# Kernel tuning notes

Measured on AMD Instinct MI355X. Metric: run time of the kernel, lower is better.

Reference implementation:

```python
import jax, jax.numpy as jnp
import numpy as np

K = 5  # box-blur width along disparity axis

def _blur_disparity(x):
    # depthwise conv1d with ones(K)/K kernel, zero 'same' padding, along axis 1
    N, D, H, W = x.shape
    xp = jnp.pad(x, ((0, 0), (K // 2, K // 2), (0, 0), (0, 0)))
    acc = xp[:, 0:D]
    for s in range(1, K):
        acc = acc + xp[:, s:s + D]
    return acc / K

def _modal_mask(x):
    N, D, H, W = x.shape
    index = jnp.argmax(x, axis=1, keepdims=True)                 # [N,1,H,W] int
    d = jnp.arange(D, dtype=x.dtype).reshape(1, D, 1, 1)
    d2 = jnp.arange(D + 1, dtype=x.dtype).reshape(1, D + 1, 1, 1)
    ones = jnp.ones((N, 1, H, W), dtype=x.dtype)
    x_diff_r = jnp.diff(x, axis=1, prepend=ones, append=ones)    # [N,D+1,H,W]
    x_diff_l = jnp.diff(x, axis=1, prepend=ones)                 # [N,D,H,W]
    # right edge of dominant mode: first positive diff strictly right of peak
    ind_r = ((x_diff_r * (d2 > index)) > 0).astype(jnp.int32)
    index_r = jnp.argmax(ind_r, axis=1, keepdims=True) - 1
    # left edge: last negative diff at/left of peak
    ind_l = ((x_diff_l * (d <= index)) < 0).astype(jnp.int32)
    index_l = D - 1 - jnp.argmax(jnp.flip(ind_l, axis=1), axis=1, keepdims=True)
    mask1 = (d >= index_l) & (d <= index_r)
    r = jnp.minimum(index_r - index, index - index_l)
    mask2 = (d >= index - r) & (d <= index + r)
    valid = jnp.abs(2 * index - index_r - index_l) < 3           # near-symmetric mode
    return jnp.where(valid, mask1, mask2)                        # bool [N,D,H,W]

def setup_inputs() -> dict:
    key = jax.random.key(0)
    N, D, H, W = 2, 192, 256, 512
    x = jax.random.uniform(key, (N, D, H, W), dtype=jnp.float32)
    return {"x": x}

def reference(x) -> jnp.ndarray:
    N, D, H, W = x.shape
    disp = jnp.arange(D, dtype=x.dtype).reshape(1, D, 1, 1)
    x_blur = _blur_disparity(x)
    mask = _modal_mask(x_blur)
    y = x * mask                       # primary mode mass
    z = x - y
    x_blur2 = x_blur * (~mask)
    z = z * _modal_mask(x_blur2)       # secondary mode mass
    valid = (jnp.sum(y, axis=1) >= jnp.sum(z, axis=1)).astype(jnp.float32)[:, None]
    xm = valid * y + (1.0 - valid) * z
    xm = xm / jnp.sum(xm, axis=1, keepdims=True)
    out = jnp.sum(xm * disp, axis=1, keepdims=True)  # [N,1,H,W]
    return out
```

## Files before the change

### kernel.cpp

```cpp
#include <hip/hip_runtime.h>
#include <math.h>

namespace {
constexpr int D     = 192;
constexpr int HW    = 256 * 512;
constexpr int TOTAL = 2 * HW;

__device__ __forceinline__ float div5(float s) {
    const float c = 0.2f;
    float q = s * c;
    float r = __builtin_fmaf(-5.0f, q, s);
    return __builtin_fmaf(r, c, q);
}

__device__ __forceinline__ bool in_range(int d, int lo, unsigned width) {
    return (unsigned)(d - lo) <= width;
}

struct Machine {
    float bprev, maxv;
    int   index, last_fall, index_l, index_r;
    bool  r_found;

    __device__ __forceinline__ void init() {
        bprev = 1.0f;
        maxv  = -INFINITY;
        index = 0; last_fall = 0; index_l = 0;
        index_r = D - 1;
        r_found = false;
    }

    __device__ __forceinline__ void step(int d, float b) {
        float diff = b - bprev;
        bool fall  = diff < 0.0f;
        last_fall  = fall ? d : last_fall;
        bool am    = b > maxv;
        maxv       = am ? b : maxv;
        index      = am ? d : index;
        index_l    = am ? last_fall : index_l;
        bool rise  = (diff > 0.0f) & (!r_found) & (!am);
        index_r    = am ? (D - 1) : (rise ? (d - 1) : index_r);
        r_found    = am ? false : (r_found | rise);
        bprev      = b;
    }

    __device__ __forceinline__ void finish(int& lo, unsigned& wd) const {
        int r = min(index_r - index, index - index_l);
        int t = 2 * index - index_r - index_l;
        bool valid = (t > -3) && (t < 3);
        lo = valid ? index_l : (index - r);
        int hi = valid ? index_r : (index + r);
        wd = (unsigned)(hi - lo);
    }
};

template<int OFS>
__device__ __forceinline__ void loadc(const float* __restrict__ col, int c,
                                      float (&buf)[8]) {
    #pragma unroll
    for (int j = 0; j < 8; ++j)
        buf[j] = col[(size_t)(8 * c + OFS + j) * HW];
}
template<int OFS>
__device__ __forceinline__ void loadc_guard(const float* __restrict__ col, int c,
                                            float (&buf)[8]) {
    #pragma unroll
    for (int j = 0; j < 8; ++j) {
        int idx = 8 * c + OFS + j;
        buf[j] = (idx < D) ? col[(size_t)idx * HW] : 0.0f;
    }
}

template<int OFS, typename F>
__device__ __forceinline__ void stream24(const float* __restrict__ col, F&& f) {
    float A[8], B[8], C[8];
    loadc<OFS>(col, 0, A);
    loadc<OFS>(col, 1, B);
    loadc<OFS>(col, 2, C);
    int d = 0;
    auto comp = [&](float (&buf)[8]) {
        #pragma unroll
        for (int j = 0; j < 8; ++j) { f(d, buf[j]); ++d; }
    };
    for (int g = 0; g < 6; ++g) {
        comp(A); loadc<OFS>(col, 3 * g + 3, A);
        comp(B); loadc<OFS>(col, 3 * g + 4, B);
        comp(C); loadc<OFS>(col, 3 * g + 5, C);
    }
    comp(A); loadc<OFS>(col, 21, A);
    comp(B); loadc<OFS>(col, 22, B);
    comp(C);
    if (OFS == 2) loadc_guard<OFS>(col, 23, C);
    else          loadc<OFS>(col, 23, C);
    comp(A); comp(B); comp(C);
}
}

extern "C" __global__ void __launch_bounds__(256, 4)
dme_kernel(const float* __restrict__ x, float* __restrict__ out)
{
    const int n  = blockIdx.x >> 9;
    const int hw = ((blockIdx.x & 511) << 8) | threadIdx.x;
    const float* __restrict__ col = x + (size_t)n * (size_t)(D * HW) + hw;

    const float x0 = col[0];
    const float x1 = col[HW];

    Machine m1; m1.init();
    {
        float w0 = 0.f, w1 = 0.f, w2 = x0, w3 = x1;
        stream24<2>(col, [&](int d, float xv) {
            float s = w0 + w1; s += w2; s += w3; s += xv;
            m1.step(d, div5(s));
            w0 = w1; w1 = w2; w2 = w3; w3 = xv;
        });
    }
    int lo1; unsigned wd1; m1.finish(lo1, wd1);

    Machine m2; m2.init();
    float sum_y = 0.f, wsum_y = 0.f;
    {
        float w0 = 0.f, w1 = 0.f, w2 = x0, w3 = x1;
        float fd = 0.0f;
        stream24<2>(col, [&](int d, float xv) {
            float s = w0 + w1; s += w2; s += w3; s += xv;
            float b = div5(s);
            bool in1 = in_range(d, lo1, wd1);
            m2.step(d, in1 ? 0.0f : b);
            sum_y += in1 ? w2 : 0.f;
            float t = in1 ? fd : 0.f;
            wsum_y = __builtin_fmaf(t, w2, wsum_y);
            w0 = w1; w1 = w2; w2 = w3; w3 = xv; fd += 1.0f;
        });
    }
    int lo2; unsigned wd2; m2.finish(lo2, wd2);

    float sum_z = 0.f, wsum_z = 0.f;
    {
        float fd = 0.0f;
        stream24<0>(col, [&](int d, float xv) {
            bool z = in_range(d, lo2, wd2) & !in_range(d, lo1, wd1);
            sum_z += z ? xv : 0.f;
            float t = z ? fd : 0.f;
            wsum_z = __builtin_fmaf(t, xv, wsum_z);
            fd += 1.0f;
        });
    }

    bool  v = (sum_y >= sum_z);
    float S = v ? sum_y  : sum_z;
    float W = v ? wsum_y : wsum_z;
    out[hw + n * HW] = W / S;
}

extern "C" void kernel_launch(void* const* d_in, const int* in_sizes, int n_in,
                              void* d_out, int out_size, void* d_ws, size_t ws_size,
                              hipStream_t stream)
{
    const float* x   = (const float*)d_in[0];
    float*       out = (float*)d_out;
    dim3 block(256), grid(TOTAL / 256);
    hipLaunchKernelGGL(dme_kernel, grid, block, 0, stream, x, out);
}
```

Baseline: 323.6 us.

## Split disparity axis across two threads per pixel with shared-memory state merge

Each pixel is now handled by two threads, one scanning disparities 0-95 and the other 96-191. Each pass runs a partial argmax/edge state machine, and the halves are merged through shared memory with __syncthreads. The aim is to halve the serial dependency chain per thread and double the grid size to expose more parallelism and latency hiding. Launch bounds rise to 8 blocks/SM and addressing moves to 32-bit byte offsets. The cost is extra shared memory traffic, barriers, and fragile merge logic for edge detection across the split point.

```diff
diff --git a/kernel.cpp b/kernel.cpp
--- a/kernel.cpp
+++ b/kernel.cpp
@@ -5,6 +5,7 @@
 constexpr int D     = 192;
 constexpr int HW    = 256 * 512;
 constexpr int TOTAL = 2 * HW;
+constexpr unsigned ROWB = (unsigned)HW * 4u;
 
 __device__ __forceinline__ float div5(float s) {
     const float c = 0.2f;
@@ -13,23 +14,31 @@
     return __builtin_fmaf(r, c, q);
 }
 
-__device__ __forceinline__ bool in_range(int d, int lo, unsigned width) {
-    return (unsigned)(d - lo) <= width;
-}
-
-struct Machine {
+__device__ __forceinline__ float ldx(const float* __restrict__ xn, unsigned bo) {
+    return *reinterpret_cast<const float*>(
+               reinterpret_cast<const char*>(xn) + bo);
+}
+
+__device__ __forceinline__ bool in_range(int d, int lo, unsigned wd) {
+    return (unsigned)(d - lo) <= wd;
+}
+
+struct Mach {
     float bprev, maxv;
-    int   index, last_fall, index_l, index_r;
+    int   index, last_fall, index_l, index_r, fra;
     bool  r_found;
 
-    __device__ __forceinline__ void init() {
-        bprev = 1.0f;
-        maxv  = -INFINITY;
-        index = 0; last_fall = 0; index_l = 0;
-        index_r = D - 1;
-        r_found = false;
-    }
-
+    __device__ __forceinline__ void initA() {
+        bprev = 1.0f; maxv = -INFINITY;
+        index = 0; last_fall = 0; index_l = 0; index_r = D - 1;
+        fra = D; r_found = false;
+    }
+    __device__ __forceinline__ void initB(float seed) {
+        bprev = seed; maxv = -INFINITY;
+        index = 96; last_fall = -1; index_l = -1; index_r = D - 1;
+        fra = D; r_found = false;
+    }
+    template<bool UP>
     __device__ __forceinline__ void step(int d, float b) {
         float diff = b - bprev;
         bool fall  = diff < 0.0f;
@@ -41,116 +50,196 @@
         bool rise  = (diff > 0.0f) & (!r_found) & (!am);
         index_r    = am ? (D - 1) : (rise ? (d - 1) : index_r);
         r_found    = am ? false : (r_found | rise);
-        bprev      = b;
-    }
-
-    __device__ __forceinline__ void finish(int& lo, unsigned& wd) const {
-        int r = min(index_r - index, index - index_l);
-        int t = 2 * index - index_r - index_l;
-        bool valid = (t > -3) && (t < 3);
-        lo = valid ? index_l : (index - r);
-        int hi = valid ? index_r : (index + r);
-        wd = (unsigned)(hi - lo);
+        if (UP) fra = min(fra, (diff > 0.0f) ? d : D);
+        bprev = b;
     }
 };
 
-template<int OFS>
-__device__ __forceinline__ void loadc(const float* __restrict__ col, int c,
-                                      float (&buf)[8]) {
+template<int NG>
+__device__ __forceinline__ void ld8(const float* __restrict__ xn, unsigned vo4,
+                                    int c, float (&buf)[8]) {
     #pragma unroll
     for (int j = 0; j < 8; ++j)
-        buf[j] = col[(size_t)(8 * c + OFS + j) * HW];
-}
-template<int OFS>
-__device__ __forceinline__ void loadc_guard(const float* __restrict__ col, int c,
-                                            float (&buf)[8]) {
-    #pragma unroll
-    for (int j = 0; j < 8; ++j) {
-        int idx = 8 * c + OFS + j;
-        buf[j] = (idx < D) ? col[(size_t)idx * HW] : 0.0f;
-    }
-}
-
-template<int OFS, typename F>
-__device__ __forceinline__ void stream24(const float* __restrict__ col, F&& f) {
+        buf[j] = (j < NG) ? ldx(xn, vo4 + (unsigned)(8 * c + j) * ROWB) : 0.0f;
+}
+
+template<int LASTN, typename F>
+__device__ __forceinline__ void stream12(const float* __restrict__ xn,
+                                         unsigned vo4, int d0, F&& f) {
     float A[8], B[8], C[8];
-    loadc<OFS>(col, 0, A);
-    loadc<OFS>(col, 1, B);
-    loadc<OFS>(col, 2, C);
-    int d = 0;
+    ld8<8>(xn, vo4, 0, A);
+    ld8<8>(xn, vo4, 1, B);
+    ld8<8>(xn, vo4, 2, C);
+    int d = d0;
     auto comp = [&](float (&buf)[8]) {
         #pragma unroll
         for (int j = 0; j < 8; ++j) { f(d, buf[j]); ++d; }
     };
-    for (int g = 0; g < 6; ++g) {
-        comp(A); loadc<OFS>(col, 3 * g + 3, A);
-        comp(B); loadc<OFS>(col, 3 * g + 4, B);
-        comp(C); loadc<OFS>(col, 3 * g + 5, C);
-    }
-    comp(A); loadc<OFS>(col, 21, A);
-    comp(B); loadc<OFS>(col, 22, B);
-    comp(C);
-    if (OFS == 2) loadc_guard<OFS>(col, 23, C);
-    else          loadc<OFS>(col, 23, C);
+    comp(A); ld8<8>(xn, vo4, 3, A);
+    comp(B); ld8<8>(xn, vo4, 4, B);
+    comp(C); ld8<8>(xn, vo4, 5, C);
+    comp(A); ld8<8>(xn, vo4, 6, A);
+    comp(B); ld8<8>(xn, vo4, 7, B);
+    comp(C); ld8<8>(xn, vo4, 8, C);
+    comp(A); ld8<8>(xn, vo4, 9, A);
+    comp(B); ld8<8>(xn, vo4, 10, B);
+    comp(C); ld8<LASTN>(xn, vo4, 11, C);
     comp(A); comp(B); comp(C);
 }
-}
-
-extern "C" __global__ void __launch_bounds__(256, 4)
+
+template<bool UP, bool SECOND>
+__device__ __forceinline__ void blur_pass(const float* __restrict__ xn,
+        unsigned hw4, const float (&pro)[5], int lo1, unsigned wd1,
+        Mach& m, float& sum_y, float& wsum_y)
+{
+    constexpr int BASE  = UP ? 98 : 2;
+    constexpr int D0    = UP ? 96 : 0;
+    constexpr int LASTN = UP ? 6 : 8;
+    float w0, w1, w2, w3;
+    if (UP) { w0 = pro[1]; w1 = pro[2]; w2 = pro[3]; w3 = pro[4]; }
+    else    { w0 = 0.0f;   w1 = 0.0f;   w2 = pro[0]; w3 = pro[1]; }
+    if (UP) {
+        float s = pro[0] + pro[1]; s += pro[2]; s += pro[3]; s += pro[4];
+        float b95 = div5(s);
+        if (SECOND) b95 = in_range(95, lo1, wd1) ? 0.0f : b95;
+        m.initB(b95);
+    } else {
+        m.initA();
+    }
+    unsigned vo4 = hw4 + (unsigned)BASE * ROWB;
+    stream12<LASTN>(xn, vo4, D0, [&](int d, float xv) {
+        float s = w0 + w1; s += w2; s += w3; s += xv;
+        float b = div5(s);
+        if (SECOND) {
+            bool in1 = in_range(d, lo1, wd1);
+            float xm = in1 ? w2 : 0.0f;
+            sum_y += xm;
+            wsum_y = __builtin_fmaf(xm, (float)d, wsum_y);
+            b = in1 ? 0.0f : b;
+        }
+        m.template step<UP>(d, b);
+        w0 = w1; w1 = w2; w2 = w3; w3 = xv;
+    });
+}
+
+template<bool UP>
+__device__ __forceinline__ void z_pass(const float* __restrict__ xn,
+        unsigned hw4, int lo1, unsigned wd1, int lo2, unsigned wd2,
+        float& sz, float& wz)
+{
+    constexpr int BASE = UP ? 96 : 0;
+    unsigned vo4 = hw4 + (unsigned)BASE * ROWB;
+    stream12<8>(xn, vo4, BASE, [&](int d, float xv) {
+        bool z = in_range(d, lo2, wd2) & !in_range(d, lo1, wd1);
+        float xm = z ? xv : 0.0f;
+        sz += xm;
+        wz = __builtin_fmaf(xm, (float)d, wz);
+    });
+}
+
+__device__ __forceinline__ void merge_finish(
+        float Amax, int Aidx, int Ail, int Alf, int Air, int Arf,
+        float Bmax, int Bidx, int Bil, int Bir, int Bfra,
+        int& lo, unsigned& wd)
+{
+    bool bw = Bmax > Amax;
+    int index   = bw ? Bidx : Aidx;
+    int index_l = bw ? (Bil >= 0 ? Bil : Alf)
+                     : Ail;
+    int index_r = bw ? Bir
+                     : (Arf ? Air
+                            : ((Bfra < D) ? (Bfra - 1) : (D - 1)));
+    int r  = min(index_r - index, index - index_l);
+    int t  = 2 * index - index_r - index_l;
+    bool valid = (t > -3) && (t < 3);
+    lo = valid ? index_l : (index - r);
+    int hi = valid ? index_r : (index + r);
+    wd = (unsigned)(hi - lo);
+}
+}
+
+extern "C" __global__ void __launch_bounds__(256, 8)
 dme_kernel(const float* __restrict__ x, float* __restrict__ out)
 {
-    const int n  = blockIdx.x >> 9;
-    const int hw = ((blockIdx.x & 511) << 8) | threadIdx.x;
-    const float* __restrict__ col = x + (size_t)n * (size_t)(D * HW) + hw;
-
-    const float x0 = col[0];
-    const float x1 = col[HW];
-
-    Machine m1; m1.init();
+    __shared__ float sAmax[2][128], sBmax[2][128];
+    __shared__ int   sAidx[2][128], sAil[2][128], sAlf[2][128],
+                     sAir[2][128],  sArf[2][128];
+    __shared__ int   sBidx[2][128], sBil[2][128], sBir[2][128], sBfra[2][128];
+    __shared__ float sSum[4][128];
+
+    const int  tid = threadIdx.x;
+    const bool UPT = tid >= 128;
+    const int  pix = tid & 127;
+    const int  n   = blockIdx.x >> 10;
+    const int  hw  = ((blockIdx.x & 1023) << 7) | pix;
+    const float* __restrict__ xn = x + (size_t)n * ((size_t)D * HW);
+    const unsigned hw4 = (unsigned)hw * 4u;
+
+    float pro[5];
     {
-        float w0 = 0.f, w1 = 0.f, w2 = x0, w3 = x1;
-        stream24<2>(col, [&](int d, float xv) {
-            float s = w0 + w1; s += w2; s += w3; s += xv;
-            m1.step(d, div5(s));
-            w0 = w1; w1 = w2; w2 = w3; w3 = xv;
-        });
-    }
-    int lo1; unsigned wd1; m1.finish(lo1, wd1);
-
-    Machine m2; m2.init();
-    float sum_y = 0.f, wsum_y = 0.f;
-    {
-        float w0 = 0.f, w1 = 0.f, w2 = x0, w3 = x1;
-        float fd = 0.0f;
-        stream24<2>(col, [&](int d, float xv) {
-            float s = w0 + w1; s += w2; s += w3; s += xv;
-            float b = div5(s);
-            bool in1 = in_range(d, lo1, wd1);
-            m2.step(d, in1 ? 0.0f : b);
-            sum_y += in1 ? w2 : 0.f;
-            float t = in1 ? fd : 0.f;
-            wsum_y = __builtin_fmaf(t, w2, wsum_y);
-            w0 = w1; w1 = w2; w2 = w3; w3 = xv; fd += 1.0f;
-        });
-    }
-    int lo2; unsigned wd2; m2.finish(lo2, wd2);
-
-    float sum_z = 0.f, wsum_z = 0.f;
-    {
-        float fd = 0.0f;
-        stream24<0>(col, [&](int d, float xv) {
-            bool z = in_range(d, lo2, wd2) & !in_range(d, lo1, wd1);
-            sum_z += z ? xv : 0.f;
-            float t = z ? fd : 0.f;
-            wsum_z = __builtin_fmaf(t, xv, wsum_z);
-            fd += 1.0f;
-        });
-    }
-
-    bool  v = (sum_y >= sum_z);
-    float S = v ? sum_y  : sum_z;
-    float W = v ? wsum_y : wsum_z;
-    out[hw + n * HW] = W / S;
+        const int pb = UPT ? 93 : 0;
+        unsigned bo = hw4 + (unsigned)pb * ROWB;
+        #pragma unroll
+        for (int k = 0; k < 5; ++k) pro[k] = ldx(xn, bo + (unsigned)k * ROWB);
+    }
+
+    Mach m1; float dum0 = 0.f, dum1 = 0.f;
+    if (UPT) blur_pass<true , false>(xn, hw4, pro, 0, 0u, m1, dum0, dum1);
+    else     blur_pass<false, false>(xn, hw4, pro, 0, 0u, m1, dum0, dum1);
+
+    if (!UPT) {
+        sAmax[0][pix] = m1.maxv;    sAidx[0][pix] = m1.index;
+        sAil [0][pix] = m1.index_l; sAlf [0][pix] = m1.last_fall;
+        sAir [0][pix] = m1.index_r; sArf [0][pix] = m1.r_found ? 1 : 0;
+    } else {
+        sBmax[0][pix] = m1.maxv;    sBidx[0][pix] = m1.index;
+        sBil [0][pix] = m1.index_l; sBir [0][pix] = m1.index_r;
+        sBfra[0][pix] = m1.fra;
+    }
+    __syncthreads();
+    int lo1; unsigned wd1;
+    merge_finish(sAmax[0][pix], sAidx[0][pix], sAil[0][pix], sAlf[0][pix],
+                 sAir[0][pix], sArf[0][pix],
+                 sBmax[0][pix], sBidx[0][pix], sBil[0][pix], sBir[0][pix],
+                 sBfra[0][pix], lo1, wd1);
+
+    Mach m2; float sy = 0.f, wy = 0.f;
+    if (UPT) blur_pass<true , true>(xn, hw4, pro, lo1, wd1, m2, sy, wy);
+    else     blur_pass<false, true>(xn, hw4, pro, lo1, wd1, m2, sy, wy);
+
+    if (!UPT) {
+        sAmax[1][pix] = m2.maxv;    sAidx[1][pix] = m2.index;
+        sAil [1][pix] = m2.index_l; sAlf [1][pix] = m2.last_fall;
+        sAir [1][pix] = m2.index_r; sArf [1][pix] = m2.r_found ? 1 : 0;
+    } else {
+        sBmax[1][pix] = m2.maxv;    sBidx[1][pix] = m2.index;
+        sBil [1][pix] = m2.index_l; sBir [1][pix] = m2.index_r;
+        sBfra[1][pix] = m2.fra;
+    }
+    __syncthreads();
+    int lo2; unsigned wd2;
+    merge_finish(sAmax[1][pix], sAidx[1][pix], sAil[1][pix], sAlf[1][pix],
+                 sAir[1][pix], sArf[1][pix],
+                 sBmax[1][pix], sBidx[1][pix], sBil[1][pix], sBir[1][pix],
+                 sBfra[1][pix], lo2, wd2);
+
+    float sz = 0.f, wz = 0.f;
+    if (UPT) z_pass<true >(xn, hw4, lo1, wd1, lo2, wd2, sz, wz);
+    else     z_pass<false>(xn, hw4, lo1, wd1, lo2, wd2, sz, wz);
+
+    if (!UPT) {
+        sSum[0][pix] = sy; sSum[1][pix] = wy;
+        sSum[2][pix] = sz; sSum[3][pix] = wz;
+    }
+    __syncthreads();
+    if (UPT) {
+        float SY = sSum[0][pix] + sy, WY = sSum[1][pix] + wy;
+        float SZ = sSum[2][pix] + sz, WZ = sSum[3][pix] + wz;
+        bool  v = SY >= SZ;
+        float S = v ? SY : SZ;
+        float W = v ? WY : WZ;
+        out[(size_t)n * HW + hw] = W / S;
+    }
 }
 
 extern "C" void kernel_launch(void* const* d_in, const int* in_sizes, int n_in,
@@ -159,6 +248,6 @@
 {
     const float* x   = (const float*)d_in[0];
     float*       out = (float*)d_out;
-    dim3 block(256), grid(TOTAL / 256);
+    dim3 block(256), grid(TOTAL / 128);
     hipLaunchKernelGGL(dme_kernel, grid, block, 0, stream, x, out);
 }
```

Measured after the change: 395.9 us. +22.4%, slower.

## Deepen load pipeline to six buffers and use 32-bit byte offsets

Applied to the files above, without the earlier changes.

The streaming loop over the disparity axis now keeps six 8-element register buffers in flight instead of three, and is fully unrolled. The aim is to hide more global-memory latency per thread. Addresses are computed as 32-bit byte offsets from a per-batch base pointer rather than 64-bit index multiplies, which cuts address arithmetic. The disparity weight is now a compile-time constant instead of a running float counter. The extra 24 live registers may lower occupancy under the 256x4 launch bounds or cause spills.

```diff
diff --git a/kernel.cpp b/kernel.cpp
--- a/kernel.cpp
+++ b/kernel.cpp
@@ -5,6 +5,7 @@
 constexpr int D     = 192;
 constexpr int HW    = 256 * 512;
 constexpr int TOTAL = 2 * HW;
+constexpr unsigned ROWB = (unsigned)HW * 4u;
 
 __device__ __forceinline__ float div5(float s) {
     const float c = 0.2f;
@@ -13,8 +14,13 @@
     return __builtin_fmaf(r, c, q);
 }
 
-__device__ __forceinline__ bool in_range(int d, int lo, unsigned width) {
-    return (unsigned)(d - lo) <= width;
+__device__ __forceinline__ float ldx(const float* __restrict__ xn, unsigned bo) {
+    return *reinterpret_cast<const float*>(
+               reinterpret_cast<const char*>(xn) + bo);
+}
+
+__device__ __forceinline__ bool in_range(int d, int lo, unsigned wd) {
+    return (unsigned)(d - lo) <= wd;
 }
 
 struct Machine {
@@ -54,45 +60,48 @@
     }
 };
 
-template<int OFS>
-__device__ __forceinline__ void loadc(const float* __restrict__ col, int c,
-                                      float (&buf)[8]) {
+template<int NG>
+__device__ __forceinline__ void ld8(const float* __restrict__ xn, unsigned vo4,
+                                    int c, float (&buf)[8]) {
     #pragma unroll
     for (int j = 0; j < 8; ++j)
-        buf[j] = col[(size_t)(8 * c + OFS + j) * HW];
-}
-template<int OFS>
-__device__ __forceinline__ void loadc_guard(const float* __restrict__ col, int c,
-                                            float (&buf)[8]) {
-    #pragma unroll
-    for (int j = 0; j < 8; ++j) {
-        int idx = 8 * c + OFS + j;
-        buf[j] = (idx < D) ? col[(size_t)idx * HW] : 0.0f;
-    }
+        buf[j] = (j < NG) ? ldx(xn, vo4 + (unsigned)(8 * c + j) * ROWB) : 0.0f;
 }
 
-template<int OFS, typename F>
-__device__ __forceinline__ void stream24(const float* __restrict__ col, F&& f) {
-    float A[8], B[8], C[8];
-    loadc<OFS>(col, 0, A);
-    loadc<OFS>(col, 1, B);
-    loadc<OFS>(col, 2, C);
+template<int LASTN, typename F>
+__device__ __forceinline__ void stream24(const float* __restrict__ xn,
+                                         unsigned vo4, F&& f) {
+    float A[8], B[8], C[8], Dv[8], E[8], Fv[8];
+    ld8<8>(xn, vo4, 0, A);
+    ld8<8>(xn, vo4, 1, B);
+    ld8<8>(xn, vo4, 2, C);
+    ld8<8>(xn, vo4, 3, Dv);
+    ld8<8>(xn, vo4, 4, E);
+    ld8<8>(xn, vo4, 5, Fv);
     int d = 0;
     auto comp = [&](float (&buf)[8]) {
         #pragma unroll
         for (int j = 0; j < 8; ++j) { f(d, buf[j]); ++d; }
     };
-    for (int g = 0; g < 6; ++g) {
-        comp(A); loadc<OFS>(col, 3 * g + 3, A);
-        comp(B); loadc<OFS>(col, 3 * g + 4, B);
-        comp(C); loadc<OFS>(col, 3 * g + 5, C);
-    }
-    comp(A); loadc<OFS>(col, 21, A);
-    comp(B); loadc<OFS>(col, 22, B);
-    comp(C);
-    if (OFS == 2) loadc_guard<OFS>(col, 23, C);
-    else          loadc<OFS>(col, 23, C);
-    comp(A); comp(B); comp(C);
+    comp(A);  ld8<8>(xn, vo4, 6, A);
+    comp(B);  ld8<8>(xn, vo4, 7, B);
+    comp(C);  ld8<8>(xn, vo4, 8, C);
+    comp(Dv); ld8<8>(xn, vo4, 9, Dv);
+    comp(E);  ld8<8>(xn, vo4, 10, E);
+    comp(Fv); ld8<8>(xn, vo4, 11, Fv);
+    comp(A);  ld8<8>(xn, vo4, 12, A);
+    comp(B);  ld8<8>(xn, vo4, 13, B);
+    comp(C);  ld8<8>(xn, vo4, 14, C);
+    comp(Dv); ld8<8>(xn, vo4, 15, Dv);
+    comp(E);  ld8<8>(xn, vo4, 16, E);
+    comp(Fv); ld8<8>(xn, vo4, 17, Fv);
+    comp(A);  ld8<8>(xn, vo4, 18, A);
+    comp(B);  ld8<8>(xn, vo4, 19, B);
+    comp(C);  ld8<8>(xn, vo4, 20, C);
+    comp(Dv); ld8<8>(xn, vo4, 21, Dv);
+    comp(E);  ld8<8>(xn, vo4, 22, E);
+    comp(Fv); ld8<LASTN>(xn, vo4, 23, Fv);
+    comp(A); comp(B); comp(C); comp(Dv); comp(E); comp(Fv);
 }
 }
 
@@ -101,15 +110,16 @@
 {
     const int n  = blockIdx.x >> 9;
     const int hw = ((blockIdx.x & 511) << 8) | threadIdx.x;
-    const float* __restrict__ col = x + (size_t)n * (size_t)(D * HW) + hw;
+    const float* __restrict__ xn = x + (size_t)n * ((size_t)D * HW);
+    const unsigned hw4 = (unsigned)hw * 4u;
 
-    const float x0 = col[0];
-    const float x1 = col[HW];
+    const float x0 = ldx(xn, hw4);
+    const float x1 = ldx(xn, hw4 + ROWB);
 
     Machine m1; m1.init();
     {
         float w0 = 0.f, w1 = 0.f, w2 = x0, w3 = x1;
-        stream24<2>(col, [&](int d, float xv) {
+        stream24<6>(xn, hw4 + 2u * ROWB, [&](int d, float xv) {
             float s = w0 + w1; s += w2; s += w3; s += xv;
             m1.step(d, div5(s));
             w0 = w1; w1 = w2; w2 = w3; w3 = xv;
@@ -121,29 +131,26 @@
     float sum_y = 0.f, wsum_y = 0.f;
     {
         float w0 = 0.f, w1 = 0.f, w2 = x0, w3 = x1;
-        float fd = 0.0f;
-        stream24<2>(col, [&](int d, float xv) {
+        stream24<6>(xn, hw4 + 2u * ROWB, [&](int d, float xv) {
             float s = w0 + w1; s += w2; s += w3; s += xv;
             float b = div5(s);
             bool in1 = in_range(d, lo1, wd1);
             m2.step(d, in1 ? 0.0f : b);
-            sum_y += in1 ? w2 : 0.f;
-            float t = in1 ? fd : 0.f;
-            wsum_y = __builtin_fmaf(t, w2, wsum_y);
-            w0 = w1; w1 = w2; w2 = w3; w3 = xv; fd += 1.0f;
+            float xm = in1 ? w2 : 0.0f;
+            sum_y += xm;
+            wsum_y = __builtin_fmaf(xm, (float)d, wsum_y);
+            w0 = w1; w1 = w2; w2 = w3; w3 = xv;
         });
     }
     int lo2; unsigned wd2; m2.finish(lo2, wd2);
 
     float sum_z = 0.f, wsum_z = 0.f;
     {
-        float fd = 0.0f;
-        stream24<0>(col, [&](int d, float xv) {
+        stream24<8>(xn, hw4, [&](int d, float xv) {
             bool z = in_range(d, lo2, wd2) & !in_range(d, lo1, wd1);
-            sum_z += z ? xv : 0.f;
-            float t = z ? fd : 0.f;
-            wsum_z = __builtin_fmaf(t, xv, wsum_z);
-            fd += 1.0f;
+            float xm = z ? xv : 0.0f;
+            sum_z += xm;
+            wsum_z = __builtin_fmaf(xm, (float)d, wsum_z);
         });
     }
 
```

New measurement: 460.8 us. 1.42x slower.
